# Kernel tuning notes

Hardware: AMD Instinct MI355X
Metric: run time of the kernel (lower is better)

## Reference

```python
import jax, jax.numpy as jnp
import numpy as np

N_INT4, N_INT8, K, GROUP = 6144, 2048, 8192, 128
N_TOTAL = N_INT4 + N_INT8
M = 16


def setup_inputs() -> dict:
    key = jax.random.key(0)
    ks = jax.random.split(key, 8)
    x = jax.random.normal(ks[0], (M, K), jnp.float32)
    # uint4 weights: values 0..15 (stored int32)
    w_int4 = jax.random.randint(ks[1], (N_INT4, K), 0, 16, jnp.int32)
    # group-wise scales [N_int4, K//group_size]
    s_int4 = jax.random.uniform(ks[2], (N_INT4, K // GROUP), jnp.float32, minval=0.005, maxval=0.02)
    # int8 weights stored in offset-128 form (w_int8 + 128 -> 0..255), as pack_for_marlin builds
    w_uint8 = jax.random.randint(ks[3], (N_INT8, K), 0, 256, jnp.int32)
    # per-channel int8 scales
    s_int8 = jax.random.uniform(ks[4], (N_INT8,), jnp.float32, minval=0.005, maxval=0.02)
    awq_scales = jax.random.uniform(ks[5], (K,), jnp.float32, minval=0.5, maxval=2.0)
    bias = jax.random.normal(ks[6], (N_TOTAL,), jnp.float32) * 0.01
    inv_perm = jax.random.permutation(ks[7], N_TOTAL).astype(jnp.int32)
    return dict(x=x, w_int4=w_int4, s_int4=s_int4, w_uint8=w_uint8, s_int8=s_int8,
                awq_scales=awq_scales, bias=bias, inv_perm=inv_perm, group_size=GROUP)


def reference(x, w_int4, s_int4, w_uint8, s_int8, awq_scales, bias, inv_perm, group_size):
    dt = x.dtype
    k = x.shape[-1]
    # AWQ input scaling (unfused path: x / awq_scales)
    x2 = x.reshape(-1, k) / awq_scales[None, :]
    sum_x = jnp.sum(x2, axis=1, keepdims=True)  # [M, 1]

    # Marlin uint4b8 dequant: (q - 8) * scale, group-wise scales for int4 rows
    s4_k = jnp.repeat(s_int4, group_size, axis=1)            # [N4, K]
    W4 = (w_int4.astype(dt) - 8.0) * s4_k                    # [N4, K]

    # int8 rows split into high/low nibbles with scales 16*s and s
    high = (w_uint8 >> 4) & 15
    low = w_uint8 & 15
    Wh = (high.astype(dt) - 8.0) * (16.0 * s_int8)[:, None]  # [N8, K]
    Wl = (low.astype(dt) - 8.0) * s_int8[:, None]            # [N8, K]

    Wc = jnp.concatenate([W4, Wh, Wl], axis=0)               # [N4+2*N8, K]
    y = x2 @ Wc.T                                            # marlin_gemm equivalent

    n4 = W4.shape[0]
    n8 = s_int8.shape[0]
    y4 = y[:, :n4]
    # int8 reconstruction: y_high + y_low + 8*s_int8*sum_x  == s_int8 * (x @ w_int8^T)
    y8 = y[:, n4:n4 + n8] + y[:, n4 + n8:] + (8.0 * s_int8)[None, :] * sum_x
    y_out = jnp.concatenate([y4, y8], axis=-1)[:, inv_perm] + bias[None, :]
    return y_out.reshape(*x.shape[:-1], n4 + n8)
```

## Files before the change

### kernel.cpp

```cpp
#include <hip/hip_runtime.h>
#include <hip/hip_bf16.h>

constexpr int K    = 8192;
constexpr int N4   = 6144;
constexpr int N8   = 2048;
constexpr int NT   = N4 + N8;
constexpr int NG   = K / 128;

typedef short  short8  __attribute__((ext_vector_type(8)));
typedef float  floatx4 __attribute__((ext_vector_type(4)));

__device__ inline short f2bf(float f) {
    __hip_bfloat16 h = __float2bfloat16(f);
    return __builtin_bit_cast(short, h);
}

__global__ void prep_kernel(const float* __restrict__ x,
                            const float* __restrict__ awq,
                            const int*   __restrict__ inv_perm,
                            short* __restrict__ x2bf,
                            int*   __restrict__ fwd) {
    const int tid  = blockIdx.x * blockDim.x + threadIdx.x;
    const int c    = tid >> 9;
    const int rem  = tid & 511;
    const int lane = rem >> 3;
    const int j    = rem & 7;
    const int m    = lane & 15;
    const int k    = c * 32 + (lane >> 4) * 8 + j;
    x2bf[tid] = f2bf(x[m * K + k] / awq[k]);
    if (tid < NT) fwd[inv_perm[tid]] = tid;
}

__global__ __launch_bounds__(256)
void qgemv_kernel(const short* __restrict__ xf,
                  const int*   __restrict__ w4,
                  const float* __restrict__ s4,
                  const int*   __restrict__ w8,
                  const float* __restrict__ s8,
                  const int*   __restrict__ fwd,
                  const float* __restrict__ bias,
                  float* __restrict__ out) {
    __shared__ float lds[4 * 256];

    const int t    = threadIdx.x;
    const int lane = t & 63;
    const int w    = t >> 6;
    const int nb   = blockIdx.x * 16;
    const int i    = lane & 15;
    const int q    = lane >> 4;
    const int row  = nb + i;

    const bool is4 = (nb < N4);
    const int*   wp = (is4 ? (w4 + (size_t)row * K)
                           : (w8 + (size_t)(row - N4) * K))
                      + (size_t)w * 2048 + q * 8;
    const short* xw = xf + (size_t)w * 64 * 512 + lane * 8;
    const float* sp = is4 ? (s4 + (size_t)row * NG + w * 16) : nullptr;

    floatx4 acc = {0.f, 0.f, 0.f, 0.f};

    int4   wbA[8], wbB[8];
    short8 abA[4], abB[4];
    float  sA = 0.f, sB = 0.f;

    auto loadg = [&](int g, int4* wb, short8* ab, float& s) {
        #pragma unroll
        for (int c = 0; c < 4; ++c) {
            const size_t co = (size_t)(g * 4 + c);
            wb[2 * c]     = *(const int4*)(wp + co * 32);
            wb[2 * c + 1] = *(const int4*)(wp + co * 32 + 4);
            ab[c]         = *(const short8*)(xw + co * 512);
        }
        if (is4) s = sp[g];
    };

    auto compg = [&](const int4* wb, const short8* ab, float s) {
        const float sc = is4 ? s : 1.f;
        const float sb = is4 ? -8.f * s : -128.f;
        #pragma unroll
        for (int c = 0; c < 4; ++c) {
            const int4 wa = wb[2 * c];
            const int4 wz = wb[2 * c + 1];
            short8 bf;
            bf[0] = f2bf((float)wa.x * sc + sb);
            bf[1] = f2bf((float)wa.y * sc + sb);
            bf[2] = f2bf((float)wa.z * sc + sb);
            bf[3] = f2bf((float)wa.w * sc + sb);
            bf[4] = f2bf((float)wz.x * sc + sb);
            bf[5] = f2bf((float)wz.y * sc + sb);
            bf[6] = f2bf((float)wz.z * sc + sb);
            bf[7] = f2bf((float)wz.w * sc + sb);
            acc = __builtin_amdgcn_mfma_f32_16x16x32_bf16(ab[c], bf, acc, 0, 0, 0);
        }
    };

    loadg(0, wbA, abA, sA);
    #pragma unroll 1
    for (int g = 0; g < 16; g += 2) {
        const int g1 = (g + 1 < 16) ? g + 1 : 15;
        loadg(g1, wbB, abB, sB);
        compg(wbA, abA, sA);
        const int g2 = (g + 2 < 16) ? g + 2 : 15;
        loadg(g2, wbA, abA, sA);
        compg(wbB, abB, sB);
    }

    #pragma unroll
    for (int r = 0; r < 4; ++r)
        lds[w * 256 + (q * 4 + r) * 16 + i] = acc[r];
    __syncthreads();

    {
        const int m  = t >> 4;
        const int i2 = t & 15;
        const float v = lds[0 * 256 + t] + lds[1 * 256 + t]
                      + lds[2 * 256 + t] + lds[3 * 256 + t];
        const int n  = nb + i2;
        const float sc = is4 ? 1.f : s8[n - N4];
        const int d  = fwd[n];
        out[(size_t)m * NT + d] = v * sc + bias[d];
    }
}

extern "C" void kernel_launch(void* const* d_in, const int* in_sizes, int n_in,
                              void* d_out, int out_size, void* d_ws, size_t ws_size,
                              hipStream_t stream) {
    const float* x        = (const float*)d_in[0];
    const int*   w_int4   = (const int*)  d_in[1];
    const float* s_int4   = (const float*)d_in[2];
    const int*   w_uint8  = (const int*)  d_in[3];
    const float* s_int8   = (const float*)d_in[4];
    const float* awq      = (const float*)d_in[5];
    const float* bias     = (const float*)d_in[6];
    const int*   inv_perm = (const int*)  d_in[7];

    short* x2bf = (short*)d_ws;
    int*   fwd  = (int*)((char*)d_ws + (size_t)16 * K * sizeof(short));

    prep_kernel<<<(16 * K) / 256, 256, 0, stream>>>(x, awq, inv_perm, x2bf, fwd);
    qgemv_kernel<<<NT / 16, 256, 0, stream>>>(x2bf, w_int4, s_int4,
                                              w_uint8, s_int8, fwd, bias,
                                              (float*)d_out);
}
```

Baseline: 337.9 us.

## Split K across two blocks per tile with atomic accumulation and prep-time bias init

Each 16-row tile is now handled by two blocks, each covering half of K. The second step reduces through atomicAdd into an output that prep_kernel pre-fills with bias. This doubles the grid from 512 to 1024 blocks to put more loads in flight on a memory-bound GEMV. The change also adds sched_barrier hints to keep the software pipeline's loads ahead of compute, and a launch-bounds occupancy hint. The cost is float atomics on the output, which make summation order nondeterministic, plus extra output traffic.

Result: no change. 336.7 us (-0.4%).

```diff
diff --git a/kernel.cpp b/kernel.cpp
--- a/kernel.cpp
+++ b/kernel.cpp
@@ -6,6 +6,7 @@
 constexpr int N8   = 2048;
 constexpr int NT   = N4 + N8;
 constexpr int NG   = K / 128;
+constexpr int KS   = 4096;
 
 typedef short  short8  __attribute__((ext_vector_type(8)));
 typedef float  floatx4 __attribute__((ext_vector_type(4)));
@@ -18,8 +19,10 @@
 __global__ void prep_kernel(const float* __restrict__ x,
                             const float* __restrict__ awq,
                             const int*   __restrict__ inv_perm,
+                            const float* __restrict__ bias,
                             short* __restrict__ x2bf,
-                            int*   __restrict__ fwd) {
+                            int*   __restrict__ fwd,
+                            float* __restrict__ out) {
     const int tid  = blockIdx.x * blockDim.x + threadIdx.x;
     const int c    = tid >> 9;
     const int rem  = tid & 511;
@@ -29,33 +32,36 @@
     const int k    = c * 32 + (lane >> 4) * 8 + j;
     x2bf[tid] = f2bf(x[m * K + k] / awq[k]);
     if (tid < NT) fwd[inv_perm[tid]] = tid;
+    out[tid] = bias[tid & (NT - 1)];
 }
 
-__global__ __launch_bounds__(256)
+__global__ __launch_bounds__(256, 4)
 void qgemv_kernel(const short* __restrict__ xf,
                   const int*   __restrict__ w4,
                   const float* __restrict__ s4,
                   const int*   __restrict__ w8,
                   const float* __restrict__ s8,
                   const int*   __restrict__ fwd,
-                  const float* __restrict__ bias,
                   float* __restrict__ out) {
     __shared__ float lds[4 * 256];
 
-    const int t    = threadIdx.x;
-    const int lane = t & 63;
-    const int w    = t >> 6;
-    const int nb   = blockIdx.x * 16;
-    const int i    = lane & 15;
-    const int q    = lane >> 4;
-    const int row  = nb + i;
+    const int t     = threadIdx.x;
+    const int lane  = t & 63;
+    const int w     = t >> 6;
+    const int tile  = blockIdx.x >> 1;
+    const int split = blockIdx.x & 1;
+    const int nb    = tile * 16;
+    const int i     = lane & 15;
+    const int q     = lane >> 4;
+    const int row   = nb + i;
 
-    const bool is4 = (nb < N4);
+    const bool is4  = (nb < N4);
+    const int kbase = split * KS + w * 1024;
     const int*   wp = (is4 ? (w4 + (size_t)row * K)
                            : (w8 + (size_t)(row - N4) * K))
-                      + (size_t)w * 2048 + q * 8;
-    const short* xw = xf + (size_t)w * 64 * 512 + lane * 8;
-    const float* sp = is4 ? (s4 + (size_t)row * NG + w * 16) : nullptr;
+                      + kbase + q * 8;
+    const short* xw = xf + (size_t)(kbase >> 5) * 512 + lane * 8;
+    const float* sp = is4 ? (s4 + (size_t)row * NG + (kbase >> 7)) : nullptr;
 
     floatx4 acc = {0.f, 0.f, 0.f, 0.f};
 
@@ -95,15 +101,20 @@
     };
 
     loadg(0, wbA, abA, sA);
+    __builtin_amdgcn_sched_barrier(0);
     #pragma unroll 1
-    for (int g = 0; g < 16; g += 2) {
-        const int g1 = (g + 1 < 16) ? g + 1 : 15;
-        loadg(g1, wbB, abB, sB);
+    for (int g = 0; g < 6; g += 2) {
+        loadg(g + 1, wbB, abB, sB);
+        __builtin_amdgcn_sched_barrier(0);
         compg(wbA, abA, sA);
-        const int g2 = (g + 2 < 16) ? g + 2 : 15;
-        loadg(g2, wbA, abA, sA);
+        loadg(g + 2, wbA, abA, sA);
+        __builtin_amdgcn_sched_barrier(0);
         compg(wbB, abB, sB);
     }
+    loadg(7, wbB, abB, sB);
+    __builtin_amdgcn_sched_barrier(0);
+    compg(wbA, abA, sA);
+    compg(wbB, abB, sB);
 
     #pragma unroll
     for (int r = 0; r < 4; ++r)
@@ -118,7 +129,7 @@
         const int n  = nb + i2;
         const float sc = is4 ? 1.f : s8[n - N4];
         const int d  = fwd[n];
-        out[(size_t)m * NT + d] = v * sc + bias[d];
+        atomicAdd(&out[(size_t)m * NT + d], v * sc);
     }
 }
 
@@ -137,8 +148,9 @@
     short* x2bf = (short*)d_ws;
     int*   fwd  = (int*)((char*)d_ws + (size_t)16 * K * sizeof(short));
 
-    prep_kernel<<<(16 * K) / 256, 256, 0, stream>>>(x, awq, inv_perm, x2bf, fwd);
-    qgemv_kernel<<<NT / 16, 256, 0, stream>>>(x2bf, w_int4, s_int4,
-                                              w_uint8, s_int8, fwd, bias,
-                                              (float*)d_out);
+    prep_kernel<<<(16 * K) / 256, 256, 0, stream>>>(x, awq, inv_perm, bias,
+                                                    x2bf, fwd, (float*)d_out);
+    qgemv_kernel<<<(NT / 16) * 2, 256, 0, stream>>>(x2bf, w_int4, s_int4,
+                                                    w_uint8, s_int8, fwd,
+                                                    (float*)d_out);
 }
```
